# Performance work log

Measured on AMD Instinct MI355X. Metric: run time of the kernel, lower is better.

Reference implementation:

```python
import jax, jax.numpy as jnp
import numpy as np

B, IN, H, A = 2048, 2048, 2048, 2
DT = 0.05
TAU = 0.05
SIGMA_V = 1.0
V_RESET = 0.0
R = 0.1
I0 = 0.7


def setup_inputs() -> dict:
    key = jax.random.key(0)
    ks = jax.random.split(key, 13)
    return {
        "x": jax.random.normal(ks[0], (B, IN), jnp.float32),
        "firing": jax.random.uniform(ks[1], (B, H), jnp.float32),
        "voltage": jax.random.normal(ks[2], (B, H), jnp.float32),
        "ascurrent": jax.random.normal(ks[3], (A, B, H), jnp.float32),
        "syncurrent": jax.random.normal(ks[4], (B, H), jnp.float32),
        "firing_delayed": jax.random.uniform(ks[5], (B, H), jnp.float32),
        "weight_iv": jax.random.normal(ks[6], (IN, H), jnp.float32) / np.sqrt(H),
        "weight_lat": jax.random.normal(ks[7], (H, H), jnp.float32) / np.sqrt(H),
        "thresh": jax.random.normal(ks[8], (1, H), jnp.float32),
        "trans_k_m": jax.random.normal(ks[9], (1, H), jnp.float32),
        "trans_k_j": jax.random.normal(ks[10], (A, 1, H), jnp.float32),
        "trans_r_j": jax.random.normal(ks[11], (A, 1, H), jnp.float32),
        "a_j": jax.random.normal(ks[12], (A, 1, H), jnp.float32),
    }


def reference(x, firing, voltage, ascurrent, syncurrent, firing_delayed,
              weight_iv, weight_lat, thresh, trans_k_m, trans_k_j, trans_r_j, a_j):
    # synaptic current: input + lateral matmuls
    syncurrent = x @ weight_iv + firing_delayed @ weight_lat  # (B, H)
    # after-spike currents (broadcast params (A,1,H) over batch)
    asc_r = 1.0 - 2.0 * jax.nn.sigmoid(trans_r_j)
    k_j = jax.nn.sigmoid(trans_k_j) / DT
    ascurrent = ((ascurrent * asc_r + a_j) * firing * (DT / TAU)
                 + (1.0 - DT * k_j) * ascurrent)  # (A, B, H)
    # voltage update
    k_m = jax.nn.sigmoid(trans_k_m) / DT
    voltage = (syncurrent
               + DT * k_m * R * (jnp.sum(ascurrent, axis=0) + I0)
               + (1.0 - DT * k_m) * voltage
               - (DT / TAU) * firing * (voltage - V_RESET))
    # sigmoid spike function
    firing = jax.nn.sigmoid((voltage - thresh) / SIGMA_V)
    return (firing, voltage, ascurrent, syncurrent)
```

## Files before the change

kernel.cpp:

```cpp
#include <hip/hip_runtime.h>

typedef unsigned short u16;
typedef __bf16 __attribute__((ext_vector_type(8))) bf16x8;
typedef float __attribute__((ext_vector_type(4))) floatx4;

#define BH 4194304
#define HDIM 2048
#define KTOT 4096

__device__ __forceinline__ float bf2f(u16 u) {
  unsigned int v = ((unsigned int)u) << 16;
  return __builtin_bit_cast(float, v);
}
__device__ __forceinline__ u16 f2bf(float f) {
  unsigned int v = __builtin_bit_cast(unsigned int, f);
  unsigned int r = (v + 0x7fffu + ((v >> 16) & 1u)) >> 16;
  return (u16)r;
}
__device__ __forceinline__ unsigned cvtpk(float a, float b) {
  unsigned r;
  asm("v_cvt_pk_bf16_f32 %0, %1, %2" : "=v"(r) : "v"(a), "v"(b));
  return r;
}
__device__ __forceinline__ unsigned packu(u16 a, u16 b) {
  return (unsigned)a | ((unsigned)b << 16);
}
__device__ __forceinline__ float sigm(float x) {
  return 1.f / (1.f + __expf(-x));
}

template <bool F32> struct Elt { using T = float; };
template <> struct Elt<false> { using T = u16; };

template <bool F32> struct Stage;
template <> struct Stage<true>  { float4 a[4]; float b[16]; };
template <> struct Stage<false> { uint4  a[2]; u16   b[16]; };

template <bool F32>
__device__ __forceinline__ float ldel(const void* p, size_t i) {
  if constexpr (F32) return ((const float*)p)[i];
  else return bf2f(((const u16*)p)[i]);
}
template <bool F32>
__device__ __forceinline__ void stel(void* p, size_t i, float v) {
  if constexpr (F32) ((float*)p)[i] = v;
  else ((u16*)p)[i] = f2bf(v);
}

template <bool F32>
__device__ void glifr_body(
    const void* xv, const void* fdv, const void* wivv, const void* wlatv,
    const void* firingv, const void* voltagev, const void* ascv,
    const void* threshv, const void* tkmv, const void* tkjv,
    const void* trjv, const void* ajv, void* outv,
    u16* As, u16* Bs) {
  using El = typename Elt<F32>::T;
  const El* x    = (const El*)xv;
  const El* fd   = (const El*)fdv;
  const El* wiv  = (const El*)wivv;
  const El* wlat = (const El*)wlatv;

  const int tid  = threadIdx.x;
  const int lane = tid & 63;
  const int w    = tid >> 6;
  const int wm   = w >> 1;
  const int wn   = w & 1;
  const int m0   = blockIdx.y * 64;
  const int n0   = blockIdx.x * 64;

  int rowA[2], dgA[2];
#pragma unroll
  for (int i = 0; i < 2; ++i) {
    int slot = tid + i * 256;
    rowA[i] = slot >> 3;
    dgA[i]  = slot & 7;
  }
  const int quad  = lane >> 4;
  const int col   = lane & 15;
  const int kbase = w * 16;

  floatx4 acc[2][2] = {};
  Stage<F32> st;

#pragma unroll
  for (int i = 0; i < 2; ++i) {
    const El* p = x + (size_t)(m0 + rowA[i]) * HDIM + dgA[i] * 8;
    if constexpr (F32) {
      st.a[2 * i]     = *(const float4*)p;
      st.a[2 * i + 1] = *(const float4*)(p + 4);
    } else {
      st.a[i] = *(const uint4*)p;
    }
  }
  {
    const El* p = wiv + (size_t)kbase * HDIM + n0 + lane;
#pragma unroll
    for (int j = 0; j < 16; ++j) st.b[j] = p[(size_t)j * HDIM];
  }

  for (int kb = 0; kb < KTOT; kb += 64) {
#pragma unroll
    for (int i = 0; i < 2; ++i) {
      uint4 q;
      if constexpr (F32) {
        q.x = cvtpk(st.a[2 * i].x, st.a[2 * i].y);
        q.y = cvtpk(st.a[2 * i].z, st.a[2 * i].w);
        q.z = cvtpk(st.a[2 * i + 1].x, st.a[2 * i + 1].y);
        q.w = cvtpk(st.a[2 * i + 1].z, st.a[2 * i + 1].w);
      } else {
        q = st.a[i];
      }
      *(uint4*)&As[rowA[i] * 64 + ((dgA[i] ^ (rowA[i] & 7)) << 3)] = q;
    }
#pragma unroll
    for (int c = 0; c < 2; ++c) {
      uint4 q;
      if constexpr (F32) {
        q.x = cvtpk(st.b[8 * c + 0], st.b[8 * c + 1]);
        q.y = cvtpk(st.b[8 * c + 2], st.b[8 * c + 3]);
        q.z = cvtpk(st.b[8 * c + 4], st.b[8 * c + 5]);
        q.w = cvtpk(st.b[8 * c + 6], st.b[8 * c + 7]);
      } else {
        q.x = packu(st.b[8 * c + 0], st.b[8 * c + 1]);
        q.y = packu(st.b[8 * c + 2], st.b[8 * c + 3]);
        q.z = packu(st.b[8 * c + 4], st.b[8 * c + 5]);
        q.w = packu(st.b[8 * c + 6], st.b[8 * c + 7]);
      }
      const int ch = 2 * w + c;
      *(uint4*)&Bs[lane * 64 + ((ch ^ (lane & 7)) << 3)] = q;
    }

    if (kb + 64 < KTOT) {
      const int kn = kb + 64;
      const El* asrc = (kn < 2048) ? (x + kn) : (fd + (kn - 2048));
      const El* wsrc = (kn < 2048) ? (wiv + (size_t)kn * HDIM)
                                   : (wlat + (size_t)(kn - 2048) * HDIM);
#pragma unroll
      for (int i = 0; i < 2; ++i) {
        const El* p = asrc + (size_t)(m0 + rowA[i]) * HDIM + dgA[i] * 8;
        if constexpr (F32) {
          st.a[2 * i]     = *(const float4*)p;
          st.a[2 * i + 1] = *(const float4*)(p + 4);
        } else {
          st.a[i] = *(const uint4*)p;
        }
      }
      const El* p = wsrc + (size_t)kbase * HDIM + n0 + lane;
#pragma unroll
      for (int j = 0; j < 16; ++j) st.b[j] = p[(size_t)j * HDIM];
    }
    __syncthreads();

#pragma unroll
    for (int kk = 0; kk < 64; kk += 32) {
      bf16x8 a[2], b[2];
#pragma unroll
      for (int mi = 0; mi < 2; ++mi) {
        const int r = wm * 32 + mi * 16 + col;
        const int p = ((kk >> 3) + quad) ^ (r & 7);
        a[mi] = *(const bf16x8*)&As[r * 64 + p * 8];
      }
#pragma unroll
      for (int ni = 0; ni < 2; ++ni) {
        const int r = wn * 32 + ni * 16 + col;
        const int p = ((kk >> 3) + quad) ^ (r & 7);
        b[ni] = *(const bf16x8*)&Bs[r * 64 + p * 8];
      }
#pragma unroll
      for (int mi = 0; mi < 2; ++mi)
#pragma unroll
        for (int ni = 0; ni < 2; ++ni)
          acc[mi][ni] = __builtin_amdgcn_mfma_f32_16x16x32_bf16(
              a[mi], b[ni], acc[mi][ni], 0, 0, 0);
    }
    __syncthreads();
  }

#pragma unroll
  for (int ni = 0; ni < 2; ++ni) {
    const int h = n0 + wn * 32 + ni * 16 + col;
    const float th  = ldel<F32>(threshv, h);
    const float sm  = sigm(ldel<F32>(tkmv, h));
    const float sk0 = sigm(ldel<F32>(tkjv, h));
    const float sk1 = sigm(ldel<F32>(tkjv, HDIM + h));
    const float r0  = 1.f - 2.f * sigm(ldel<F32>(trjv, h));
    const float r1  = 1.f - 2.f * sigm(ldel<F32>(trjv, HDIM + h));
    const float a0c = ldel<F32>(ajv, h);
    const float a1c = ldel<F32>(ajv, HDIM + h);
#pragma unroll
    for (int mi = 0; mi < 2; ++mi) {
#pragma unroll
      for (int i = 0; i < 4; ++i) {
        const int m = m0 + wm * 32 + mi * 16 + quad * 4 + i;
        const size_t idx = (size_t)m * HDIM + h;
        const float f   = ldel<F32>(firingv, idx);
        const float v   = ldel<F32>(voltagev, idx);
        const float A0  = ldel<F32>(ascv, idx);
        const float A1  = ldel<F32>(ascv, BH + idx);
        const float syn = acc[mi][ni][i];
        const float na0 = (A0 * r0 + a0c) * f + (1.f - sk0) * A0;
        const float na1 = (A1 * r1 + a1c) * f + (1.f - sk1) * A1;
        const float nv  = syn + sm * 0.1f * (na0 + na1 + 0.7f)
                          + (1.f - sm) * v - f * v;
        const float nf  = sigm(nv - th);
        stel<F32>(outv, idx,            nf);
        stel<F32>(outv, BH + idx,       nv);
        stel<F32>(outv, 2 * BH + idx,   na0);
        stel<F32>(outv, 3 * BH + idx,   na1);
        stel<F32>(outv, 4 * BH + idx,   syn);
      }
    }
  }
}

__device__ __forceinline__ bool detect_f32(const u16* xu) {
  bool wild = false;
  for (int i = (threadIdx.x & 63); i < 1024; i += 64) {
    const u16 u = xu[i];
    if ((u & 0x7f80u) == 0x7f80u || fabsf(bf2f(u)) > 64.f) wild = true;
  }
  return __any(wild);
}

__global__ __launch_bounds__(256, 4) void glifr_fused(
    const void* x, const void* fd, const void* wiv, const void* wlat,
    const void* firing, const void* voltage, const void* asc,
    const void* thresh, const void* tkm, const void* tkj, const void* trj,
    const void* aj, void* out) {
  __shared__ u16 As[64 * 64];
  __shared__ u16 Bs[64 * 64];
  if (detect_f32((const u16*)x)) {
    glifr_body<true>(x, fd, wiv, wlat, firing, voltage, asc, thresh, tkm,
                     tkj, trj, aj, out, As, Bs);
  } else {
    glifr_body<false>(x, fd, wiv, wlat, firing, voltage, asc, thresh, tkm,
                      tkj, trj, aj, out, As, Bs);
  }
}

extern "C" void kernel_launch(void* const* d_in, const int* in_sizes, int n_in,
                              void* d_out, int out_size, void* d_ws, size_t ws_size,
                              hipStream_t stream) {
  const void* x    = d_in[0];
  const void* fir  = d_in[1];
  const void* vol  = d_in[2];
  const void* asc  = d_in[3];
  const void* fd   = d_in[5];
  const void* wiv  = d_in[6];
  const void* wlat = d_in[7];
  const void* th   = d_in[8];
  const void* tkm  = d_in[9];
  const void* tkj  = d_in[10];
  const void* trj  = d_in[11];
  const void* aj   = d_in[12];

  glifr_fused<<<dim3(32, 32), 256, 0, stream>>>(
      x, fd, wiv, wlat, fir, vol, asc, th, tkm, tkj, trj, aj, d_out);
}
```

Baseline: 350.8 us.

## Double-buffer LDS tiles with two-deep prefetch, vectorize B loads, remap blocks

The K loop now uses two LDS buffers and two register staging sets. Global loads run two tiles ahead, and each iteration needs only one barrier instead of two. B-tile loads become 2-element vector loads per lane with a repacked LDS write, cutting scalar global loads. The 1D grid uses a block-index remap that groups blocks into a new order, likely for L2 or XCD locality. In exchange, LDS use doubles and register pressure rises, which may lower occupancy.

```diff
diff --git a/kernel.cpp b/kernel.cpp
--- a/kernel.cpp
+++ b/kernel.cpp
@@ -22,8 +22,8 @@
   asm("v_cvt_pk_bf16_f32 %0, %1, %2" : "=v"(r) : "v"(a), "v"(b));
   return r;
 }
-__device__ __forceinline__ unsigned packu(u16 a, u16 b) {
-  return (unsigned)a | ((unsigned)b << 16);
+__device__ __forceinline__ unsigned packu(unsigned lo, unsigned hi) {
+  return (lo & 0xffffu) | (hi << 16);
 }
 __device__ __forceinline__ float sigm(float x) {
   return 1.f / (1.f + __expf(-x));
@@ -32,9 +32,9 @@
 template <bool F32> struct Elt { using T = float; };
 template <> struct Elt<false> { using T = u16; };
 
-template <bool F32> struct Stage;
-template <> struct Stage<true>  { float4 a[4]; float b[16]; };
-template <> struct Stage<false> { uint4  a[2]; u16   b[16]; };
+template <bool F32> struct Stg;
+template <> struct Stg<true>  { float4 a[4]; float2 b[8]; };
+template <> struct Stg<false> { uint4  a[2]; unsigned b[8]; };
 
 template <bool F32>
 __device__ __forceinline__ float ldel(const void* p, size_t i) {
@@ -53,7 +53,7 @@
     const void* firingv, const void* voltagev, const void* ascv,
     const void* threshv, const void* tkmv, const void* tkjv,
     const void* trjv, const void* ajv, void* outv,
-    u16* As, u16* Bs) {
+    u16* As0, u16* Bs0, u16* As1, u16* Bs1) {
   using El = typename Elt<F32>::T;
   const El* x    = (const El*)xv;
   const El* fd   = (const El*)fdv;
@@ -65,8 +65,11 @@
   const int w    = tid >> 6;
   const int wm   = w >> 1;
   const int wn   = w & 1;
-  const int m0   = blockIdx.y * 64;
-  const int n0   = blockIdx.x * 64;
+
+  const int b   = blockIdx.x;
+  const int lin = (b & 7) * 128 + (b >> 3);
+  const int m0  = (lin >> 5) * 64;
+  const int n0  = (lin & 31) * 64;
 
   int rowA[2], dgA[2];
 #pragma unroll
@@ -75,30 +78,36 @@
     rowA[i] = slot >> 3;
     dgA[i]  = slot & 7;
   }
-  const int quad  = lane >> 4;
-  const int col   = lane & 15;
-  const int kbase = w * 16;
+  const int quad = lane >> 4;
+  const int col  = lane & 15;
+  const int kb8  = w * 16 + (lane >> 5) * 8;
+  const int chB  = w * 2 + (lane >> 5);
+  const int ne   = 2 * (lane & 31);
 
   floatx4 acc[2][2] = {};
-  Stage<F32> st;
-
-#pragma unroll
-  for (int i = 0; i < 2; ++i) {
-    const El* p = x + (size_t)(m0 + rowA[i]) * HDIM + dgA[i] * 8;
-    if constexpr (F32) {
-      st.a[2 * i]     = *(const float4*)p;
-      st.a[2 * i + 1] = *(const float4*)(p + 4);
-    } else {
-      st.a[i] = *(const uint4*)p;
-    }
-  }
-  {
-    const El* p = wiv + (size_t)kbase * HDIM + n0 + lane;
-#pragma unroll
-    for (int j = 0; j < 16; ++j) st.b[j] = p[(size_t)j * HDIM];
-  }
-
-  for (int kb = 0; kb < KTOT; kb += 64) {
+  Stg<F32> S0, S1;
+
+  auto issueA = [&](Stg<F32>& st, const El* asrc) {
+#pragma unroll
+    for (int i = 0; i < 2; ++i) {
+      const El* p = asrc + (size_t)(m0 + rowA[i]) * HDIM + dgA[i] * 8;
+      if constexpr (F32) {
+        st.a[2 * i]     = *(const float4*)p;
+        st.a[2 * i + 1] = *(const float4*)(p + 4);
+      } else {
+        st.a[i] = *(const uint4*)p;
+      }
+    }
+  };
+  auto issueB = [&](Stg<F32>& st, const El* wsrc) {
+    const El* p = wsrc + (size_t)kb8 * HDIM + n0 + ne;
+#pragma unroll
+    for (int j = 0; j < 8; ++j) {
+      if constexpr (F32) st.b[j] = *(const float2*)(p + (size_t)j * HDIM);
+      else               st.b[j] = *(const unsigned*)(p + (size_t)j * HDIM);
+    }
+  };
+  auto writeTile = [&](Stg<F32>& st, u16* As, u16* Bs) {
 #pragma unroll
     for (int i = 0; i < 2; ++i) {
       uint4 q;
@@ -112,68 +121,81 @@
       }
       *(uint4*)&As[rowA[i] * 64 + ((dgA[i] ^ (rowA[i] & 7)) << 3)] = q;
     }
-#pragma unroll
-    for (int c = 0; c < 2; ++c) {
-      uint4 q;
-      if constexpr (F32) {
-        q.x = cvtpk(st.b[8 * c + 0], st.b[8 * c + 1]);
-        q.y = cvtpk(st.b[8 * c + 2], st.b[8 * c + 3]);
-        q.z = cvtpk(st.b[8 * c + 4], st.b[8 * c + 5]);
-        q.w = cvtpk(st.b[8 * c + 6], st.b[8 * c + 7]);
-      } else {
-        q.x = packu(st.b[8 * c + 0], st.b[8 * c + 1]);
-        q.y = packu(st.b[8 * c + 2], st.b[8 * c + 3]);
-        q.z = packu(st.b[8 * c + 4], st.b[8 * c + 5]);
-        q.w = packu(st.b[8 * c + 6], st.b[8 * c + 7]);
-      }
-      const int ch = 2 * w + c;
-      *(uint4*)&Bs[lane * 64 + ((ch ^ (lane & 7)) << 3)] = q;
-    }
-
-    if (kb + 64 < KTOT) {
-      const int kn = kb + 64;
-      const El* asrc = (kn < 2048) ? (x + kn) : (fd + (kn - 2048));
-      const El* wsrc = (kn < 2048) ? (wiv + (size_t)kn * HDIM)
-                                   : (wlat + (size_t)(kn - 2048) * HDIM);
-#pragma unroll
-      for (int i = 0; i < 2; ++i) {
-        const El* p = asrc + (size_t)(m0 + rowA[i]) * HDIM + dgA[i] * 8;
-        if constexpr (F32) {
-          st.a[2 * i]     = *(const float4*)p;
-          st.a[2 * i + 1] = *(const float4*)(p + 4);
-        } else {
-          st.a[i] = *(const uint4*)p;
-        }
-      }
-      const El* p = wsrc + (size_t)kbase * HDIM + n0 + lane;
-#pragma unroll
-      for (int j = 0; j < 16; ++j) st.b[j] = p[(size_t)j * HDIM];
-    }
-    __syncthreads();
-
+    uint4 qe, qo;
+    if constexpr (F32) {
+      qe.x = cvtpk(st.b[0].x, st.b[1].x);
+      qe.y = cvtpk(st.b[2].x, st.b[3].x);
+      qe.z = cvtpk(st.b[4].x, st.b[5].x);
+      qe.w = cvtpk(st.b[6].x, st.b[7].x);
+      qo.x = cvtpk(st.b[0].y, st.b[1].y);
+      qo.y = cvtpk(st.b[2].y, st.b[3].y);
+      qo.z = cvtpk(st.b[4].y, st.b[5].y);
+      qo.w = cvtpk(st.b[6].y, st.b[7].y);
+    } else {
+      qe.x = packu(st.b[0], st.b[1]);
+      qe.y = packu(st.b[2], st.b[3]);
+      qe.z = packu(st.b[4], st.b[5]);
+      qe.w = packu(st.b[6], st.b[7]);
+      qo.x = (st.b[0] >> 16) | (st.b[1] & 0xffff0000u);
+      qo.y = (st.b[2] >> 16) | (st.b[3] & 0xffff0000u);
+      qo.z = (st.b[4] >> 16) | (st.b[5] & 0xffff0000u);
+      qo.w = (st.b[6] >> 16) | (st.b[7] & 0xffff0000u);
+    }
+    *(uint4*)&Bs[ne * 64 + ((chB ^ (ne & 7)) << 3)]             = qe;
+    *(uint4*)&Bs[(ne + 1) * 64 + ((chB ^ ((ne + 1) & 7)) << 3)] = qo;
+  };
+  auto mfmaPhase = [&](const u16* As, const u16* Bs) {
 #pragma unroll
     for (int kk = 0; kk < 64; kk += 32) {
-      bf16x8 a[2], b[2];
+      bf16x8 af[2], bf[2];
 #pragma unroll
       for (int mi = 0; mi < 2; ++mi) {
         const int r = wm * 32 + mi * 16 + col;
         const int p = ((kk >> 3) + quad) ^ (r & 7);
-        a[mi] = *(const bf16x8*)&As[r * 64 + p * 8];
+        af[mi] = *(const bf16x8*)&As[r * 64 + p * 8];
       }
 #pragma unroll
       for (int ni = 0; ni < 2; ++ni) {
         const int r = wn * 32 + ni * 16 + col;
         const int p = ((kk >> 3) + quad) ^ (r & 7);
-        b[ni] = *(const bf16x8*)&Bs[r * 64 + p * 8];
+        bf[ni] = *(const bf16x8*)&Bs[r * 64 + p * 8];
       }
 #pragma unroll
       for (int mi = 0; mi < 2; ++mi)
 #pragma unroll
         for (int ni = 0; ni < 2; ++ni)
           acc[mi][ni] = __builtin_amdgcn_mfma_f32_16x16x32_bf16(
-              a[mi], b[ni], acc[mi][ni], 0, 0, 0);
-    }
-    __syncthreads();
+              af[mi], bf[ni], acc[mi][ni], 0, 0, 0);
+    }
+  };
+  auto srcA = [&](int kn) -> const El* {
+    return (kn < 2048) ? (x + kn) : (fd + (kn - 2048));
+  };
+  auto srcW = [&](int kn) -> const El* {
+    return (kn < 2048) ? (wiv + (size_t)kn * HDIM)
+                       : (wlat + (size_t)(kn - 2048) * HDIM);
+  };
+
+  issueA(S0, srcA(0));   issueB(S0, srcW(0));
+  issueA(S1, srcA(64));  issueB(S1, srcW(64));
+  writeTile(S0, As0, Bs0);
+  __syncthreads();
+
+  for (int t = 0; t < 64; t += 2) {
+    {
+      const int kn = (t + 2) * 64;
+      if (kn < KTOT) { issueA(S0, srcA(kn)); issueB(S0, srcW(kn)); }
+      mfmaPhase(As0, Bs0);
+      writeTile(S1, As1, Bs1);
+      __syncthreads();
+    }
+    {
+      const int kn = (t + 3) * 64;
+      if (kn < KTOT) { issueA(S1, srcA(kn)); issueB(S1, srcW(kn)); }
+      mfmaPhase(As1, Bs1);
+      if ((t + 2) * 64 < KTOT) writeTile(S0, As0, Bs0);
+      __syncthreads();
+    }
   }
 
 #pragma unroll
@@ -227,14 +249,16 @@
     const void* firing, const void* voltage, const void* asc,
     const void* thresh, const void* tkm, const void* tkj, const void* trj,
     const void* aj, void* out) {
-  __shared__ u16 As[64 * 64];
-  __shared__ u16 Bs[64 * 64];
+  __shared__ u16 As0[64 * 64];
+  __shared__ u16 Bs0[64 * 64];
+  __shared__ u16 As1[64 * 64];
+  __shared__ u16 Bs1[64 * 64];
   if (detect_f32((const u16*)x)) {
     glifr_body<true>(x, fd, wiv, wlat, firing, voltage, asc, thresh, tkm,
-                     tkj, trj, aj, out, As, Bs);
+                     tkj, trj, aj, out, As0, Bs0, As1, Bs1);
   } else {
     glifr_body<false>(x, fd, wiv, wlat, firing, voltage, asc, thresh, tkm,
-                      tkj, trj, aj, out, As, Bs);
+                      tkj, trj, aj, out, As0, Bs0, As1, Bs1);
   }
 }
 
@@ -254,6 +278,6 @@
   const void* trj  = d_in[11];
   const void* aj   = d_in[12];
 
-  glifr_fused<<<dim3(32, 32), 256, 0, stream>>>(
+  glifr_fused<<<dim3(1024), 256, 0, stream>>>(
       x, fd, wiv, wlat, fir, vol, asc, th, tkm, tkj, trj, aj, d_out);
 }
```

New measurement: 405.8 us. +15.7%, slower.
